# Performance work log

Hardware: AMD Instinct MI355X
Metric: run time of the kernel (lower is better)

The kernel has to match this reference:

```python
import jax, jax.numpy as jnp
import numpy as np

B, L, H = 32, 40, 448
S, NCAND = 8000, 25
T = S * NCAND  # 200000 total candidates


def setup_inputs() -> dict:
    key = jax.random.key(0)
    k1, k2, k3, k4, k5 = jax.random.split(key, 5)
    return {
        "x_mol_vecs": jax.random.normal(k1, (B, L, H), dtype=jnp.float32),
        "cand_vecs": jax.random.normal(k2, (T, H), dtype=jnp.float32),
        "W_assm": jax.random.normal(k3, (H, H), dtype=jnp.float32) / np.sqrt(H),
        "batch_idx": jax.random.randint(k4, (T,), 0, B),
        "label_in_seg": jax.random.randint(k5, (S,), 0, NCAND),
        "ncand": NCAND,
        "num_segments": S,
    }


def reference(x_mol_vecs, cand_vecs, W_assm, batch_idx, label_in_seg, ncand, num_segments):
    # ---- DiffVAE.assm ----
    nbatch = x_mol_vecs.shape[0]
    total = cand_vecs.shape[0]
    # x_mol_vecs.sum(dim=1) -> [B, H]; A_assm is linear so we apply it before the
    # gather (mathematically identical to index_select-then-Linear, far cheaper).
    x_pool = jnp.einsum("blh,kh->bk", x_mol_vecs, W_assm)       # [B, H] (A_assm applied)
    x_gather = x_pool[batch_idx]                                  # [T, H]
    # scores = bmm(x.unsqueeze(1), cand.unsqueeze(-1)).squeeze() -> rowwise dot
    scores = jnp.sum(x_gather * cand_vecs, axis=-1)               # [T]

    # segment structure: fixed ncand candidates per competing node
    seg_ids = jnp.arange(total) // ncand                          # [T], sorted
    label_global = jnp.arange(num_segments) * ncand + label_in_seg  # [S]

    seg_max = jax.ops.segment_max(scores, seg_ids, num_segments,
                                  indices_are_sorted=True)        # [S]
    exp_sum = jax.ops.segment_sum(jnp.exp(scores - seg_max[seg_ids]), seg_ids,
                                  num_segments, indices_are_sorted=True)
    lse = seg_max + jnp.log(exp_sum)                              # [S] log-sum-exp per segment

    label_scores = scores[label_global]                           # [S]
    # CrossEntropyLoss(size_average=False) summed over segments, / len(mol_batch)
    loss = jnp.sum(lse - label_scores) / nbatch
    # acc += 1 when label score >= segment max
    acc = jnp.mean((label_scores >= seg_max).astype(jnp.float32))
    return loss, acc
```

## Files before the change

### kernel.cpp

```cpp
#include <hip/hip_runtime.h>
#include <math.h>

#define BB 32
#define LL 40
#define HH 448
#define SS 8000
#define NC 25
#define H4 (HH / 4)
#define NBLK (SS / 4)

typedef float f4 __attribute__((ext_vector_type(4)));

__global__ __launch_bounds__(256) void pool_kernel(const float* __restrict__ x,
                                                   const float* __restrict__ W,
                                                   float* __restrict__ xpool) {
    __shared__ float xsum[HH];
    const int b = blockIdx.x;
    const int kc = blockIdx.y;
    const int tid = threadIdx.x;
    const float* xb = x + (size_t)b * LL * HH;

    for (int h = tid; h < HH; h += 256) {
        float s = 0.f;
        #pragma unroll 8
        for (int l = 0; l < LL; ++l) s += xb[(size_t)l * HH + h];
        xsum[h] = s;
    }
    __syncthreads();

    const int kk  = tid >> 2;
    const int sub = tid & 3;
    const int k   = kc * 64 + kk;
    const f4* wr = (const f4*)(W + (size_t)k * HH);
    float acc = 0.f;
    #pragma unroll 7
    for (int j = sub; j < H4; j += 4) {
        f4 w4 = wr[j];
        acc += xsum[j * 4 + 0] * w4.x;
        acc += xsum[j * 4 + 1] * w4.y;
        acc += xsum[j * 4 + 2] * w4.z;
        acc += xsum[j * 4 + 3] * w4.w;
    }
    acc += __shfl_xor(acc, 1, 64);
    acc += __shfl_xor(acc, 2, 64);
    if (sub == 0) xpool[b * HH + k] = acc;
}

__global__ __launch_bounds__(256) void score_kernel(
        const float* __restrict__ cand,
        const float* __restrict__ xpool,
        const int* __restrict__ batch_idx,
        const int* __restrict__ label_in_seg,
        float* __restrict__ blk_loss,
        float* __restrict__ blk_acc) {
    __shared__ float s_loss[4];
    __shared__ float s_acc[4];
    const int wave = threadIdx.x >> 6;
    const int lane = threadIdx.x & 63;
    const int seg = blockIdx.x * 4 + wave;

    const int label = label_in_seg[seg];
    const long t0 = (long)seg * NC;

    float m = -INFINITY;
    float ssum = 0.f;
    float label_score = 0.f;

    for (int c = 0; c < NC; ++c) {
        const long t = t0 + c;
        const int bi = batch_idx[t];
        const f4* cr = (const f4*)(cand + t * (long)HH);
        const f4* xr = (const f4*)(xpool + bi * HH);

        f4 a = __builtin_nontemporal_load(cr + lane);
        f4 b = xr[lane];
        float p = a.x * b.x + a.y * b.y + a.z * b.z + a.w * b.w;
        if (lane < 48) {
            f4 a2 = __builtin_nontemporal_load(cr + 64 + lane);
            f4 b2 = xr[64 + lane];
            p += a2.x * b2.x + a2.y * b2.y + a2.z * b2.z + a2.w * b2.w;
        }

        #pragma unroll
        for (int off = 32; off > 0; off >>= 1) p += __shfl_xor(p, off, 64);

        const float score = p;
        if (c == label) label_score = score;
        const float nm = fmaxf(m, score);
        ssum = ssum * __expf(m - nm) + __expf(score - nm);
        m = nm;
    }

    if (lane == 0) {
        const float lse = m + __logf(ssum);
        s_loss[wave] = lse - label_score;
        s_acc[wave] = (label_score >= m) ? 1.f : 0.f;
    }
    __syncthreads();
    if (threadIdx.x == 0) {
        blk_loss[blockIdx.x] = (s_loss[0] + s_loss[1]) + (s_loss[2] + s_loss[3]);
        blk_acc[blockIdx.x]  = (s_acc[0] + s_acc[1]) + (s_acc[2] + s_acc[3]);
    }
}

__global__ __launch_bounds__(256) void reduce_kernel(const float* __restrict__ blk_loss,
                                                     const float* __restrict__ blk_acc,
                                                     float* __restrict__ out) {
    __shared__ float sl[256];
    __shared__ float sa[256];
    const int tid = threadIdx.x;
    float l = 0.f, a = 0.f;
    for (int s = tid; s < NBLK; s += 256) {
        l += blk_loss[s];
        a += blk_acc[s];
    }
    sl[tid] = l;
    sa[tid] = a;
    __syncthreads();
    for (int off = 128; off > 0; off >>= 1) {
        if (tid < off) {
            sl[tid] += sl[tid + off];
            sa[tid] += sa[tid + off];
        }
        __syncthreads();
    }
    if (tid == 0) {
        out[0] = sl[0] / (float)BB;
        out[1] = sa[0] / (float)SS;
    }
}

extern "C" void kernel_launch(void* const* d_in, const int* in_sizes, int n_in,
                              void* d_out, int out_size, void* d_ws, size_t ws_size,
                              hipStream_t stream) {
    const float* x_mol   = (const float*)d_in[0];
    const float* cand    = (const float*)d_in[1];
    const float* W       = (const float*)d_in[2];
    const int*   bidx    = (const int*)d_in[3];
    const int*   label   = (const int*)d_in[4];
    float* out = (float*)d_out;

    float* ws       = (float*)d_ws;
    float* xpool    = ws;
    float* blk_loss = ws + BB * HH;
    float* blk_acc  = blk_loss + NBLK;

    dim3 pgrid(BB, 7);
    pool_kernel<<<pgrid, 256, 0, stream>>>(x_mol, W, xpool);
    score_kernel<<<NBLK, 256, 0, stream>>>(cand, xpool, bidx, label,
                                           blk_loss, blk_acc);
    reduce_kernel<<<1, 256, 0, stream>>>(blk_loss, blk_acc, out);
}
```

Baseline: 75.82 us.

## Batch candidate loads in chunks of five and shrink pool and reduce kernels

The score kernel now issues loads for five candidates at once before reducing, so more memory requests are in flight per wave, and it does a chunked online softmax. The pool kernel uses 8 threads per output across 14 column blocks to launch more blocks, the partial results are packed as float2, and the final reduce uses a single wave with shuffles. The chunking raises register pressure in exchange for better memory-level parallelism on the 358 MB candidate stream.

Result: slower. 81.79 us (+7.9%).

```diff
diff --git a/kernel.cpp b/kernel.cpp
--- a/kernel.cpp
+++ b/kernel.cpp
@@ -8,6 +8,7 @@
 #define NC 25
 #define H4 (HH / 4)
 #define NBLK (SS / 4)
+#define CHUNK 5
 
 typedef float f4 __attribute__((ext_vector_type(4)));
 
@@ -28,13 +29,13 @@
     }
     __syncthreads();
 
-    const int kk  = tid >> 2;
-    const int sub = tid & 3;
-    const int k   = kc * 64 + kk;
+    const int kk  = tid >> 3;
+    const int sub = tid & 7;
+    const int k   = kc * 32 + kk;
     const f4* wr = (const f4*)(W + (size_t)k * HH);
     float acc = 0.f;
-    #pragma unroll 7
-    for (int j = sub; j < H4; j += 4) {
+    #pragma unroll 14
+    for (int j = sub; j < H4; j += 8) {
         f4 w4 = wr[j];
         acc += xsum[j * 4 + 0] * w4.x;
         acc += xsum[j * 4 + 1] * w4.y;
@@ -43,6 +44,7 @@
     }
     acc += __shfl_xor(acc, 1, 64);
     acc += __shfl_xor(acc, 2, 64);
+    acc += __shfl_xor(acc, 4, 64);
     if (sub == 0) xpool[b * HH + k] = acc;
 }
 
@@ -51,8 +53,7 @@
         const float* __restrict__ xpool,
         const int* __restrict__ batch_idx,
         const int* __restrict__ label_in_seg,
-        float* __restrict__ blk_loss,
-        float* __restrict__ blk_acc) {
+        float2* __restrict__ blk_part) {
     __shared__ float s_loss[4];
     __shared__ float s_acc[4];
     const int wave = threadIdx.x >> 6;
@@ -66,29 +67,39 @@
     float ssum = 0.f;
     float label_score = 0.f;
 
-    for (int c = 0; c < NC; ++c) {
-        const long t = t0 + c;
-        const int bi = batch_idx[t];
-        const f4* cr = (const f4*)(cand + t * (long)HH);
-        const f4* xr = (const f4*)(xpool + bi * HH);
-
-        f4 a = __builtin_nontemporal_load(cr + lane);
-        f4 b = xr[lane];
-        float p = a.x * b.x + a.y * b.y + a.z * b.z + a.w * b.w;
-        if (lane < 48) {
-            f4 a2 = __builtin_nontemporal_load(cr + 64 + lane);
-            f4 b2 = xr[64 + lane];
-            p += a2.x * b2.x + a2.y * b2.y + a2.z * b2.z + a2.w * b2.w;
+    #pragma unroll 1
+    for (int cc = 0; cc < NC; cc += CHUNK) {
+        float sc[CHUNK];
+        #pragma unroll
+        for (int u = 0; u < CHUNK; ++u) {
+            const long t = t0 + cc + u;
+            const int bi = batch_idx[t];
+            const f4* cr = (const f4*)(cand + t * (long)HH);
+            const f4* xr = (const f4*)(xpool + bi * HH);
+            f4 a = __builtin_nontemporal_load(cr + lane);
+            f4 b = xr[lane];
+            float p = a.x * b.x + a.y * b.y + a.z * b.z + a.w * b.w;
+            if (lane < 48) {
+                f4 a2 = __builtin_nontemporal_load(cr + 64 + lane);
+                f4 b2 = xr[64 + lane];
+                p += a2.x * b2.x + a2.y * b2.y + a2.z * b2.z + a2.w * b2.w;
+            }
+            sc[u] = p;
         }
-
         #pragma unroll
-        for (int off = 32; off > 0; off >>= 1) p += __shfl_xor(p, off, 64);
-
-        const float score = p;
-        if (c == label) label_score = score;
-        const float nm = fmaxf(m, score);
-        ssum = ssum * __expf(m - nm) + __expf(score - nm);
+        for (int off = 32; off > 0; off >>= 1) {
+            #pragma unroll
+            for (int u = 0; u < CHUNK; ++u) sc[u] += __shfl_xor(sc[u], off, 64);
+        }
+        float cmax = fmaxf(fmaxf(fmaxf(sc[0], sc[1]), fmaxf(sc[2], sc[3])), sc[4]);
+        const float nm = fmaxf(m, cmax);
+        float add = __expf(sc[0] - nm) + __expf(sc[1] - nm) + __expf(sc[2] - nm)
+                  + __expf(sc[3] - nm) + __expf(sc[4] - nm);
+        ssum = ssum * __expf(m - nm) + add;
         m = nm;
+        #pragma unroll
+        for (int u = 0; u < CHUNK; ++u)
+            if (cc + u == label) label_score = sc[u];
     }
 
     if (lane == 0) {
@@ -98,35 +109,29 @@
     }
     __syncthreads();
     if (threadIdx.x == 0) {
-        blk_loss[blockIdx.x] = (s_loss[0] + s_loss[1]) + (s_loss[2] + s_loss[3]);
-        blk_acc[blockIdx.x]  = (s_acc[0] + s_acc[1]) + (s_acc[2] + s_acc[3]);
+        blk_part[blockIdx.x] = make_float2(
+            (s_loss[0] + s_loss[1]) + (s_loss[2] + s_loss[3]),
+            (s_acc[0] + s_acc[1]) + (s_acc[2] + s_acc[3]));
     }
 }
 
-__global__ __launch_bounds__(256) void reduce_kernel(const float* __restrict__ blk_loss,
-                                                     const float* __restrict__ blk_acc,
-                                                     float* __restrict__ out) {
-    __shared__ float sl[256];
-    __shared__ float sa[256];
-    const int tid = threadIdx.x;
+__global__ void reduce_kernel(const float2* __restrict__ blk_part,
+                              float* __restrict__ out) {
+    const int lane = threadIdx.x;
     float l = 0.f, a = 0.f;
-    for (int s = tid; s < NBLK; s += 256) {
-        l += blk_loss[s];
-        a += blk_acc[s];
+    for (int s = lane; s < NBLK; s += 64) {
+        float2 v = blk_part[s];
+        l += v.x;
+        a += v.y;
     }
-    sl[tid] = l;
-    sa[tid] = a;
-    __syncthreads();
-    for (int off = 128; off > 0; off >>= 1) {
-        if (tid < off) {
-            sl[tid] += sl[tid + off];
-            sa[tid] += sa[tid + off];
-        }
-        __syncthreads();
+    #pragma unroll
+    for (int off = 32; off > 0; off >>= 1) {
+        l += __shfl_xor(l, off, 64);
+        a += __shfl_xor(a, off, 64);
     }
-    if (tid == 0) {
-        out[0] = sl[0] / (float)BB;
-        out[1] = sa[0] / (float)SS;
+    if (lane == 0) {
+        out[0] = l / (float)BB;
+        out[1] = a / (float)SS;
     }
 }
 
@@ -140,14 +145,12 @@
     const int*   label   = (const int*)d_in[4];
     float* out = (float*)d_out;
 
-    float* ws       = (float*)d_ws;
-    float* xpool    = ws;
-    float* blk_loss = ws + BB * HH;
-    float* blk_acc  = blk_loss + NBLK;
+    float* ws        = (float*)d_ws;
+    float* xpool     = ws;
+    float2* blk_part = (float2*)(ws + BB * HH);
 
-    dim3 pgrid(BB, 7);
+    dim3 pgrid(BB, 14);
     pool_kernel<<<pgrid, 256, 0, stream>>>(x_mol, W, xpool);
-    score_kernel<<<NBLK, 256, 0, stream>>>(cand, xpool, bidx, label,
-                                           blk_loss, blk_acc);
-    reduce_kernel<<<1, 256, 0, stream>>>(blk_loss, blk_acc, out);
+    score_kernel<<<NBLK, 256, 0, stream>>>(cand, xpool, bidx, label, blk_part);
+    reduce_kernel<<<1, 64, 0, stream>>>(blk_part, out);
 }
```
